# Optimization experiments

Measured on AMD Instinct MI355X. Metric: run time of the kernel, lower is better.

Reference implementation:

```python
import jax, jax.numpy as jnp
import numpy as np

DIM = 1024
HEADS = 16

def setup_inputs() -> dict:
    key = jax.random.key(0)
    ks = jax.random.split(key, 9)
    s = DIM ** -0.5  # init scale for weights
    x = jax.random.normal(ks[0], (2, 2048, DIM), dtype=jnp.float32)
    wq = jax.random.normal(ks[1], (DIM, DIM), dtype=jnp.float32) * s
    bq = jax.random.normal(ks[2], (DIM,), dtype=jnp.float32) * 0.01
    wk = jax.random.normal(ks[3], (DIM, DIM), dtype=jnp.float32) * s
    bk = jax.random.normal(ks[4], (DIM,), dtype=jnp.float32) * 0.01
    wv = jax.random.normal(ks[5], (DIM, DIM), dtype=jnp.float32) * s
    bv = jax.random.normal(ks[6], (DIM,), dtype=jnp.float32) * 0.01
    wo = jax.random.normal(ks[7], (DIM, DIM), dtype=jnp.float32) * s
    bo = jax.random.normal(ks[8], (DIM,), dtype=jnp.float32) * 0.01
    return {"x": x, "wq": wq, "bq": bq, "wk": wk, "bk": bk,
            "wv": wv, "bv": bv, "wo": wo, "bo": bo}

def reference(x, wq, bq, wk, bk, wv, bv, wo, bo):
    b, l, dim = x.shape
    h = HEADS
    d = dim // h
    scale = dim ** -0.5  # NOTE: full dim, as in the original module
    # torch Linear: x @ W.T + b
    def proj(w, bias):
        y = jnp.einsum('bld,ed->ble', x, w) + bias
        return y.reshape(b, l, h, d).transpose(0, 2, 1, 3)  # b h l d
    q = proj(wq, bq)
    k = proj(wk, bk)
    v = proj(wv, bv)
    attn = jnp.einsum('bhid,bhjd->bhij', q, k) * scale
    attn = jax.nn.softmax(attn, axis=-1)
    out = jnp.einsum('bhij,bhjd->bhid', attn, v)
    out = out.transpose(0, 2, 1, 3).reshape(b, l, dim)
    return jnp.einsum('ble,fe->blf', out, wo) + bo
```

## Files before the change

### kernel.cpp

```cpp
#include <hip/hip_runtime.h>
#include <hip/hip_bf16.h>
#include <stdint.h>


typedef __attribute__((ext_vector_type(8))) short short8;
typedef __attribute__((ext_vector_type(4))) float f32x4;
typedef __attribute__((ext_vector_type(16))) float f32x16;

#define MFMA(a, b, c) __builtin_amdgcn_mfma_f32_16x16x32_bf16((a), (b), (c), 0, 0, 0)
#define MFMA32(a, b, c) __builtin_amdgcn_mfma_f32_32x32x16_bf16((a), (b), (c), 0, 0, 0)

#if __has_builtin(__builtin_amdgcn_exp2f)
#define EXP2(x) __builtin_amdgcn_exp2f(x)
#else
#define EXP2(x) exp2f(x)
#endif

__device__ __forceinline__ ushort f2bf(float f) {
  uint32_t u = __builtin_bit_cast(uint32_t, f);
  u += 0x7fffu + ((u >> 16) & 1u);
  return (ushort)(u >> 16);
}

__device__ __forceinline__ uint32_t pkbf(float lo, float hi) {
  __hip_bfloat162 h = __float22bfloat162_rn(make_float2(lo, hi));
  uint32_t u;
  __builtin_memcpy(&u, &h, 4);
  return u;
}

__device__ __forceinline__ uint32_t cvtpk(float lo, float hi) {
  uint32_t u;
  asm("v_cvt_pk_bf16_f32 %0, %1, %2" : "=v"(u) : "v"(lo), "v"(hi));
  return u;
}

__device__ __forceinline__ void pl32swap(uint32_t& a, uint32_t& b) {
  asm("v_permlane32_swap_b32 %0, %1" : "+v"(a), "+v"(b));
}

__device__ __forceinline__ void gl_lds16(const void* g, void* l) {
  __builtin_amdgcn_global_load_lds(
      (const __attribute__((address_space(1))) unsigned int*)g,
      (__attribute__((address_space(3))) unsigned int*)l, 16, 0, 0);
}

__global__ __launch_bounds__(256) void convert_all(
    const float* __restrict__ x, const float* __restrict__ wq,
    const float* __restrict__ wk, const float* __restrict__ wv,
    const float* __restrict__ wo, ushort* __restrict__ dst) {
  size_t i4 = (size_t)blockIdx.x * 256 + threadIdx.x;
  size_t e = i4 * 4;
  const float* src; size_t off;
  if (e < 4194304u)      { src = x;  off = e; }
  else if (e < 5242880u) { src = wq; off = e - 4194304u; }
  else if (e < 6291456u) { src = wk; off = e - 5242880u; }
  else if (e < 7340032u) { src = wv; off = e - 6291456u; }
  else                   { src = wo; off = e - 7340032u; }
  float4 v = *(const float4*)(src + off);
  ushort4 o = { f2bf(v.x), f2bf(v.y), f2bf(v.z), f2bf(v.w) };
  *(ushort4*)(dst + e) = o;
}

__global__ __launch_bounds__(256) void gemm_qkv(
    const ushort* __restrict__ xb,
    const ushort* __restrict__ wqb, const ushort* __restrict__ wkb,
    const ushort* __restrict__ wvb,
    const float* __restrict__ bq_, const float* __restrict__ bk_,
    const float* __restrict__ bv_,
    ushort* __restrict__ qout, ushort* __restrict__ kout,
    ushort* __restrict__ vtout) {
  __shared__ __align__(16) ushort As[128 * 32];
  __shared__ __align__(16) ushort Bs[128 * 32];
  const int z = blockIdx.z;
  const int bn = blockIdx.x, bm = blockIdx.y;
  const int t = threadIdx.x;
  const int w = t >> 6, lane = t & 63;
  const int wr = w >> 1, wc = w & 1;
  const int l15 = lane & 15, l4 = lane >> 4;

  const ushort* wb = (z == 0) ? wqb : (z == 1 ? wkb : wvb);
  const float* bias = (z == 0) ? bq_ : (z == 1 ? bk_ : bv_);

  f32x4 acc[4][4] = {};

  for (int kt = 0; kt < 32; ++kt) {
    __syncthreads();
#pragma unroll
    for (int rr = 0; rr < 2; ++rr) {
      int c = t + rr * 256;
      int row = c >> 2, cin = c & 3;
      gl_lds16(xb + (bm * 128 + row) * 1024 + kt * 32 + cin * 8, (void*)&As[c * 8]);
      gl_lds16(wb + (bn * 128 + row) * 1024 + kt * 32 + cin * 8, (void*)&Bs[c * 8]);
    }
    __syncthreads();
    short8 af[4], bfr[4];
#pragma unroll
    for (int mf = 0; mf < 4; ++mf)
      af[mf] = *(const short8*)&As[(wr * 64 + mf * 16 + l15) * 32 + l4 * 8];
#pragma unroll
    for (int nf = 0; nf < 4; ++nf)
      bfr[nf] = *(const short8*)&Bs[(wc * 64 + nf * 16 + l15) * 32 + l4 * 8];
    __builtin_amdgcn_s_setprio(1);
#pragma unroll
    for (int mf = 0; mf < 4; ++mf)
#pragma unroll
      for (int nf = 0; nf < 4; ++nf)
        acc[mf][nf] = MFMA(af[mf], bfr[nf], acc[mf][nf]);
    __builtin_amdgcn_s_setprio(0);
  }

  const float qsc = 0.045084439f;
#pragma unroll
  for (int mf = 0; mf < 4; ++mf) {
#pragma unroll
    for (int nf = 0; nf < 4; ++nf) {
      int n = bn * 128 + wc * 64 + nf * 16 + l15;
      int m0 = bm * 128 + wr * 64 + mf * 16 + l4 * 4;
      float b = bias[n];
      float vals[4];
#pragma unroll
      for (int r = 0; r < 4; ++r) vals[r] = acc[mf][nf][r] + b;
      int bb = m0 >> 11, l0 = m0 & 2047;
      int h = n >> 6, d = n & 63;
      int bh = bb * 16 + h;
      if (z == 2) {
        *(uint2*)&vtout[(bh * 64 + d) * 2048 + l0] =
            make_uint2(pkbf(vals[0], vals[1]), pkbf(vals[2], vals[3]));
      } else if (z == 0) {
#pragma unroll
        for (int r = 0; r < 4; ++r)
          qout[(bh * 2048 + l0 + r) * 64 + d] = f2bf(vals[r] * qsc);
      } else {
#pragma unroll
        for (int r = 0; r < 4; ++r)
          kout[(bh * 2048 + l0 + r) * 64 + d] = f2bf(vals[r]);
      }
    }
  }
}

__global__ __launch_bounds__(256, 2) void attn(
    const ushort* __restrict__ qb, const ushort* __restrict__ kb,
    const ushort* __restrict__ vtb, ushort* __restrict__ aout) {
  __shared__ __align__(16) ushort Ks[4][64 * 64];
  __shared__ __align__(16) ushort Vs[4][64 * 64];
  const int bid = blockIdx.x;
  const int xcd = bid & 7, idx = bid >> 3;
  const int bh = xcd * 4 + (idx >> 4);
  const int it = idx & 15;
  const int t = threadIdx.x, w = t >> 6, lane = t & 63;
  const int l31 = lane & 31, hi = lane >> 5;
  const size_t kvbase = (size_t)bh * (2048 * 64);
  const int i0 = it * 128 + w * 32;

  const int c0 = t, c1 = t + 256;
  const int r0 = c0 >> 3, s0 = (c0 & 7) ^ (r0 & 7);
  const int r1 = c1 >> 3, s1 = (c1 & 7) ^ (r1 & 7);

#define STAGE(bufi, jts)                                                     \
  {                                                                          \
    const int j0s = (jts) * 64;                                              \
    gl_lds16(kb + kvbase + (size_t)(j0s + r0) * 64 + s0 * 8,                 \
             (void*)&Ks[bufi][c0 * 8]);                                      \
    gl_lds16(kb + kvbase + (size_t)(j0s + r1) * 64 + s1 * 8,                 \
             (void*)&Ks[bufi][c1 * 8]);                                      \
    gl_lds16(vtb + kvbase + (size_t)r0 * 2048 + j0s + s0 * 8,                \
             (void*)&Vs[bufi][c0 * 8]);                                      \
    gl_lds16(vtb + kvbase + (size_t)r1 * 2048 + j0s + s1 * 8,                \
             (void*)&Vs[bufi][c1 * 8]);                                      \
  }

#define QKSTEP(kbuf)                                                         \
  {                                                                          \
    const ushort* Kc = &Ks[kbuf][0];                                         \
    __builtin_amdgcn_s_setprio(1);                                           \
    _Pragma("unroll")                                                        \
    for (int ks = 0; ks < 4; ++ks) {                                         \
      int ck = (ks * 2 + hi) ^ swz;                                          \
      short8 a0 = *(const short8*)&Kc[l31 * 64 + ck * 8];                    \
      short8 a1 = *(const short8*)&Kc[(32 + l31) * 64 + ck * 8];             \
      st0 = MFMA32(a0, qf[ks], st0);                                         \
      st1 = MFMA32(a1, qf[ks], st1);                                         \
    }                                                                        \
    __builtin_amdgcn_s_setprio(0);                                           \
  }

  short8 qf[4];
#pragma unroll
  for (int ks = 0; ks < 4; ++ks)
    qf[ks] = *(const short8*)&qb[kvbase + (size_t)(i0 + l31) * 64 + ks * 16 + hi * 8];

  f32x16 ot0 = {}, ot1 = {};
  float ts0 = 0.f, ts1 = 0.f, ts2 = 0.f, ts3 = 0.f;
  const int swz = (l31 & 7);

  STAGE(0, 0);
  STAGE(1, 1);
  asm volatile("s_waitcnt vmcnt(4)" ::: "memory");
  __builtin_amdgcn_s_barrier();
  asm volatile("" ::: "memory");

  f32x16 st0 = {}, st1 = {};
  QKSTEP(0);

  for (int jt = 0; jt < 32; ++jt) {
    const int cur = jt & 3;
    STAGE((jt + 2) & 3, (jt + 2 < 32) ? (jt + 2) : 31);

    const ushort* Vc = &Vs[cur][0];
    short8 va0[4], va1[4];
#pragma unroll
    for (int b = 0; b < 4; ++b) {
      int cv = (b * 2 + hi) ^ swz;
      va0[b] = *(const short8*)&Vc[l31 * 64 + cv * 8];
      va1[b] = *(const short8*)&Vc[(32 + l31) * 64 + cv * 8];
    }

    f32x16 p0, p1;
#pragma unroll
    for (int r = 0; r < 16; r += 4) {
      p0[r] = EXP2(st0[r]);         ts0 += p0[r];
      p0[r + 1] = EXP2(st0[r + 1]); ts1 += p0[r + 1];
      p0[r + 2] = EXP2(st0[r + 2]); ts2 += p0[r + 2];
      p0[r + 3] = EXP2(st0[r + 3]); ts3 += p0[r + 3];
    }
#pragma unroll
    for (int r = 0; r < 16; r += 4) {
      p1[r] = EXP2(st1[r]);         ts0 += p1[r];
      p1[r + 1] = EXP2(st1[r + 1]); ts1 += p1[r + 1];
      p1[r + 2] = EXP2(st1[r + 2]); ts2 += p1[r + 2];
      p1[r + 3] = EXP2(st1[r + 3]); ts3 += p1[r + 3];
    }

    short8 pb[4];
#pragma unroll
    for (int b = 0; b < 4; ++b) {
      f32x16 pv = (b < 2) ? p0 : p1;
      const int R = 8 * (b & 1);
      uint32_t c01 = cvtpk(pv[R + 0], pv[R + 1]);
      uint32_t c23 = cvtpk(pv[R + 2], pv[R + 3]);
      uint32_t c45 = cvtpk(pv[R + 4], pv[R + 5]);
      uint32_t c67 = cvtpk(pv[R + 6], pv[R + 7]);
      pl32swap(c01, c45);
      pl32swap(c23, c67);
      union { uint32_t u[4]; short8 s; } pk;
      pk.u[0] = c01; pk.u[1] = c23; pk.u[2] = c45; pk.u[3] = c67;
      pb[b] = pk.s;
    }

    __builtin_amdgcn_s_setprio(1);
#pragma unroll
    for (int b = 0; b < 4; ++b) {
      ot0 = MFMA32(va0[b], pb[b], ot0);
      ot1 = MFMA32(va1[b], pb[b], ot1);
    }
    __builtin_amdgcn_s_setprio(0);

    asm volatile("s_waitcnt vmcnt(4)" ::: "memory");
    __builtin_amdgcn_s_barrier();
    asm volatile("" ::: "memory");

    if (jt < 31) {
#pragma unroll
      for (int r = 0; r < 16; ++r) { st0[r] = 0.f; st1[r] = 0.f; }
      QKSTEP((jt + 1) & 3);
    }
  }

  float lsum = (ts0 + ts1) + (ts2 + ts3);
  {
    uint32_t a = __builtin_bit_cast(uint32_t, lsum);
    uint32_t b = a;
    pl32swap(a, b);
    lsum = __builtin_bit_cast(float, a) + __builtin_bit_cast(float, b);
  }
  const int bb = bh >> 4, h = bh & 15;
  float inv = 1.0f / lsum;
  ushort* orow = aout + (size_t)(bb * 2048 + i0 + l31) * 1024 + h * 64;
#pragma unroll
  for (int mf = 0; mf < 2; ++mf) {
    f32x16 o = mf ? ot1 : ot0;
#pragma unroll
    for (int g = 0; g < 4; ++g) {
      int d0 = mf * 32 + g * 8 + hi * 4;
      *(uint2*)(orow + d0) = make_uint2(
          cvtpk(o[g * 4 + 0] * inv, o[g * 4 + 1] * inv),
          cvtpk(o[g * 4 + 2] * inv, o[g * 4 + 3] * inv));
    }
  }
#undef STAGE
#undef QKSTEP
}

__global__ __launch_bounds__(256) void gemm_out(
    const ushort* __restrict__ ab, const ushort* __restrict__ wob,
    const float* __restrict__ bo_, float* __restrict__ out) {
  __shared__ __align__(16) ushort As[128 * 32];
  __shared__ __align__(16) ushort Bs[128 * 32];
  const int bn = blockIdx.x, bm = blockIdx.y;
  const int t = threadIdx.x;
  const int w = t >> 6, lane = t & 63;
  const int wr = w >> 1, wc = w & 1;
  const int l15 = lane & 15, l4 = lane >> 4;

  f32x4 acc[4][4] = {};

  for (int kt = 0; kt < 32; ++kt) {
    __syncthreads();
#pragma unroll
    for (int rr = 0; rr < 2; ++rr) {
      int c = t + rr * 256;
      int row = c >> 2, cin = c & 3;
      gl_lds16(ab + (bm * 128 + row) * 1024 + kt * 32 + cin * 8, (void*)&As[c * 8]);
      gl_lds16(wob + (bn * 128 + row) * 1024 + kt * 32 + cin * 8, (void*)&Bs[c * 8]);
    }
    __syncthreads();
    short8 af[4], bfr[4];
#pragma unroll
    for (int mf = 0; mf < 4; ++mf)
      af[mf] = *(const short8*)&As[(wr * 64 + mf * 16 + l15) * 32 + l4 * 8];
#pragma unroll
    for (int nf = 0; nf < 4; ++nf)
      bfr[nf] = *(const short8*)&Bs[(wc * 64 + nf * 16 + l15) * 32 + l4 * 8];
    __builtin_amdgcn_s_setprio(1);
#pragma unroll
    for (int mf = 0; mf < 4; ++mf)
#pragma unroll
      for (int nf = 0; nf < 4; ++nf)
        acc[mf][nf] = MFMA(af[mf], bfr[nf], acc[mf][nf]);
    __builtin_amdgcn_s_setprio(0);
  }

#pragma unroll
  for (int mf = 0; mf < 4; ++mf)
#pragma unroll
    for (int nf = 0; nf < 4; ++nf) {
      int n = bn * 128 + wc * 64 + nf * 16 + l15;
      int m0 = bm * 128 + wr * 64 + mf * 16 + l4 * 4;
      float b = bo_[n];
#pragma unroll
      for (int r = 0; r < 4; ++r)
        out[(size_t)(m0 + r) * 1024 + n] = acc[mf][nf][r] + b;
    }
}

extern "C" void kernel_launch(void* const* d_in, const int* in_sizes, int n_in,
                              void* d_out, int out_size, void* d_ws, size_t ws_size,
                              hipStream_t stream) {
  const float* x  = (const float*)d_in[0];
  const float* wq = (const float*)d_in[1];
  const float* bq = (const float*)d_in[2];
  const float* wk = (const float*)d_in[3];
  const float* bk = (const float*)d_in[4];
  const float* wv = (const float*)d_in[5];
  const float* bv = (const float*)d_in[6];
  const float* wo = (const float*)d_in[7];
  const float* bo = (const float*)d_in[8];

  ushort* ws  = (ushort*)d_ws;
  ushort* xb  = ws;
  ushort* wqb = ws + 4194304;
  ushort* wkb = ws + 5242880;
  ushort* wvb = ws + 6291456;
  ushort* wob = ws + 7340032;
  ushort* qbp = ws + 8388608;
  ushort* kbp = ws + 12582912;
  ushort* vtb = ws + 16777216;
  ushort* ab  = ws + 20971520;

  convert_all<<<8192, 256, 0, stream>>>(x, wq, wk, wv, wo, ws);
  gemm_qkv<<<dim3(8, 32, 3), 256, 0, stream>>>(xb, wqb, wkb, wvb, bq, bk, bv,
                                               qbp, kbp, vtb);
  attn<<<512, 256, 0, stream>>>(qbp, kbp, vtb, ab);
  gemm_out<<<dim3(8, 32), 256, 0, stream>>>(ab, wob, bo, (float*)d_out);
}
```

Measured before the change: 112.6 us.

## Use 32x32 MFMA with K=64 swizzled LDS tiles in projection GEMMs

```diff
diff --git a/kernel.cpp b/kernel.cpp
--- a/kernel.cpp
+++ b/kernel.cpp
@@ -7,7 +7,6 @@
 typedef __attribute__((ext_vector_type(4))) float f32x4;
 typedef __attribute__((ext_vector_type(16))) float f32x16;
 
-#define MFMA(a, b, c) __builtin_amdgcn_mfma_f32_16x16x32_bf16((a), (b), (c), 0, 0, 0)
 #define MFMA32(a, b, c) __builtin_amdgcn_mfma_f32_32x32x16_bf16((a), (b), (c), 0, 0, 0)
 
 #if __has_builtin(__builtin_amdgcn_exp2f)
@@ -20,13 +19,6 @@
   uint32_t u = __builtin_bit_cast(uint32_t, f);
   u += 0x7fffu + ((u >> 16) & 1u);
   return (ushort)(u >> 16);
-}
-
-__device__ __forceinline__ uint32_t pkbf(float lo, float hi) {
-  __hip_bfloat162 h = __float22bfloat162_rn(make_float2(lo, hi));
-  uint32_t u;
-  __builtin_memcpy(&u, &h, 4);
-  return u;
 }
 
 __device__ __forceinline__ uint32_t cvtpk(float lo, float hi) {
@@ -70,71 +62,90 @@
     const float* __restrict__ bv_,
     ushort* __restrict__ qout, ushort* __restrict__ kout,
     ushort* __restrict__ vtout) {
-  __shared__ __align__(16) ushort As[128 * 32];
-  __shared__ __align__(16) ushort Bs[128 * 32];
+  __shared__ __align__(16) ushort As[128 * 64];
+  __shared__ __align__(16) ushort Bs[128 * 64];
   const int z = blockIdx.z;
   const int bn = blockIdx.x, bm = blockIdx.y;
   const int t = threadIdx.x;
   const int w = t >> 6, lane = t & 63;
   const int wr = w >> 1, wc = w & 1;
-  const int l15 = lane & 15, l4 = lane >> 4;
+  const int l31 = lane & 31, hi = lane >> 5;
+  const int swz = l31 & 7;
 
   const ushort* wb = (z == 0) ? wqb : (z == 1 ? wkb : wvb);
   const float* bias = (z == 0) ? bq_ : (z == 1 ? bk_ : bv_);
 
-  f32x4 acc[4][4] = {};
-
-  for (int kt = 0; kt < 32; ++kt) {
+  f32x16 acc[2][2] = {};
+
+  for (int kt = 0; kt < 16; ++kt) {
     __syncthreads();
 #pragma unroll
-    for (int rr = 0; rr < 2; ++rr) {
+    for (int rr = 0; rr < 4; ++rr) {
       int c = t + rr * 256;
-      int row = c >> 2, cin = c & 3;
-      gl_lds16(xb + (bm * 128 + row) * 1024 + kt * 32 + cin * 8, (void*)&As[c * 8]);
-      gl_lds16(wb + (bn * 128 + row) * 1024 + kt * 32 + cin * 8, (void*)&Bs[c * 8]);
+      int row = c >> 3, o = c & 7;
+      int sc = (o ^ (row & 7)) * 8;
+      gl_lds16(xb + (bm * 128 + row) * 1024 + kt * 64 + sc, (void*)&As[c * 8]);
+      gl_lds16(wb + (bn * 128 + row) * 1024 + kt * 64 + sc, (void*)&Bs[c * 8]);
     }
     __syncthreads();
-    short8 af[4], bfr[4];
-#pragma unroll
-    for (int mf = 0; mf < 4; ++mf)
-      af[mf] = *(const short8*)&As[(wr * 64 + mf * 16 + l15) * 32 + l4 * 8];
-#pragma unroll
-    for (int nf = 0; nf < 4; ++nf)
-      bfr[nf] = *(const short8*)&Bs[(wc * 64 + nf * 16 + l15) * 32 + l4 * 8];
+    short8 af[2][4], bf[2][4];
+#pragma unroll
+    for (int mb = 0; mb < 2; ++mb) {
+      int row = wr * 64 + mb * 32 + l31;
+#pragma unroll
+      for (int ks = 0; ks < 4; ++ks) {
+        int ck = (ks * 2 + hi) ^ swz;
+        af[mb][ks] = *(const short8*)&As[row * 64 + ck * 8];
+      }
+    }
+#pragma unroll
+    for (int nb = 0; nb < 2; ++nb) {
+      int row = wc * 64 + nb * 32 + l31;
+#pragma unroll
+      for (int ks = 0; ks < 4; ++ks) {
+        int ck = (ks * 2 + hi) ^ swz;
+        bf[nb][ks] = *(const short8*)&Bs[row * 64 + ck * 8];
+      }
+    }
     __builtin_amdgcn_s_setprio(1);
 #pragma unroll
-    for (int mf = 0; mf < 4; ++mf)
-#pragma unroll
-      for (int nf = 0; nf < 4; ++nf)
-        acc[mf][nf] = MFMA(af[mf], bfr[nf], acc[mf][nf]);
+    for (int ks = 0; ks < 4; ++ks)
+#pragma unroll
+      for (int mb = 0; mb < 2; ++mb)
+#pragma unroll
+        for (int nb = 0; nb < 2; ++nb)
+          acc[mb][nb] = MFMA32(af[mb][ks], bf[nb][ks], acc[mb][nb]);
     __builtin_amdgcn_s_setprio(0);
   }
 
   const float qsc = 0.045084439f;
 #pragma unroll
-  for (int mf = 0; mf < 4; ++mf) {
-#pragma unroll
-    for (int nf = 0; nf < 4; ++nf) {
-      int n = bn * 128 + wc * 64 + nf * 16 + l15;
-      int m0 = bm * 128 + wr * 64 + mf * 16 + l4 * 4;
+  for (int mb = 0; mb < 2; ++mb) {
+#pragma unroll
+    for (int nb = 0; nb < 2; ++nb) {
+      int n = bn * 128 + wc * 64 + nb * 32 + l31;
       float b = bias[n];
-      float vals[4];
-#pragma unroll
-      for (int r = 0; r < 4; ++r) vals[r] = acc[mf][nf][r] + b;
-      int bb = m0 >> 11, l0 = m0 & 2047;
       int h = n >> 6, d = n & 63;
-      int bh = bb * 16 + h;
-      if (z == 2) {
-        *(uint2*)&vtout[(bh * 64 + d) * 2048 + l0] =
-            make_uint2(pkbf(vals[0], vals[1]), pkbf(vals[2], vals[3]));
-      } else if (z == 0) {
-#pragma unroll
-        for (int r = 0; r < 4; ++r)
-          qout[(bh * 2048 + l0 + r) * 64 + d] = f2bf(vals[r] * qsc);
-      } else {
-#pragma unroll
-        for (int r = 0; r < 4; ++r)
-          kout[(bh * 2048 + l0 + r) * 64 + d] = f2bf(vals[r]);
+#pragma unroll
+      for (int g = 0; g < 4; ++g) {
+        int m0 = bm * 128 + wr * 64 + mb * 32 + g * 8 + hi * 4;
+        float vals[4];
+#pragma unroll
+        for (int e = 0; e < 4; ++e) vals[e] = acc[mb][nb][g * 4 + e] + b;
+        int bb = m0 >> 11, l0 = m0 & 2047;
+        int bh = bb * 16 + h;
+        if (z == 2) {
+          *(uint2*)&vtout[(bh * 64 + d) * 2048 + l0] =
+              make_uint2(cvtpk(vals[0], vals[1]), cvtpk(vals[2], vals[3]));
+        } else if (z == 0) {
+#pragma unroll
+          for (int e = 0; e < 4; ++e)
+            qout[(bh * 2048 + l0 + e) * 64 + d] = f2bf(vals[e] * qsc);
+        } else {
+#pragma unroll
+          for (int e = 0; e < 4; ++e)
+            kout[(bh * 2048 + l0 + e) * 64 + d] = f2bf(vals[e]);
+        }
       }
     }
   }
@@ -296,52 +307,71 @@
 __global__ __launch_bounds__(256) void gemm_out(
     const ushort* __restrict__ ab, const ushort* __restrict__ wob,
     const float* __restrict__ bo_, float* __restrict__ out) {
-  __shared__ __align__(16) ushort As[128 * 32];
-  __shared__ __align__(16) ushort Bs[128 * 32];
+  __shared__ __align__(16) ushort As[128 * 64];
+  __shared__ __align__(16) ushort Bs[128 * 64];
   const int bn = blockIdx.x, bm = blockIdx.y;
   const int t = threadIdx.x;
   const int w = t >> 6, lane = t & 63;
   const int wr = w >> 1, wc = w & 1;
-  const int l15 = lane & 15, l4 = lane >> 4;
-
-  f32x4 acc[4][4] = {};
-
-  for (int kt = 0; kt < 32; ++kt) {
+  const int l31 = lane & 31, hi = lane >> 5;
+  const int swz = l31 & 7;
+
+  f32x16 acc[2][2] = {};
+
+  for (int kt = 0; kt < 16; ++kt) {
     __syncthreads();
 #pragma unroll
-    for (int rr = 0; rr < 2; ++rr) {
+    for (int rr = 0; rr < 4; ++rr) {
       int c = t + rr * 256;
-      int row = c >> 2, cin = c & 3;
-      gl_lds16(ab + (bm * 128 + row) * 1024 + kt * 32 + cin * 8, (void*)&As[c * 8]);
-      gl_lds16(wob + (bn * 128 + row) * 1024 + kt * 32 + cin * 8, (void*)&Bs[c * 8]);
+      int row = c >> 3, o = c & 7;
+      int sc = (o ^ (row & 7)) * 8;
+      gl_lds16(ab + (bm * 128 + row) * 1024 + kt * 64 + sc, (void*)&As[c * 8]);
+      gl_lds16(wob + (bn * 128 + row) * 1024 + kt * 64 + sc, (void*)&Bs[c * 8]);
     }
     __syncthreads();
-    short8 af[4], bfr[4];
-#pragma unroll
-    for (int mf = 0; mf < 4; ++mf)
-      af[mf] = *(const short8*)&As[(wr * 64 + mf * 16 + l15) * 32 + l4 * 8];
-#pragma unroll
-    for (int nf = 0; nf < 4; ++nf)
-      bfr[nf] = *(const short8*)&Bs[(wc * 64 + nf * 16 + l15) * 32 + l4 * 8];
+    short8 af[2][4], bf[2][4];
+#pragma unroll
+    for (int mb = 0; mb < 2; ++mb) {
+      int row = wr * 64 + mb * 32 + l31;
+#pragma unroll
+      for (int ks = 0; ks < 4; ++ks) {
+        int ck = (ks * 2 + hi) ^ swz;
+        af[mb][ks] = *(const short8*)&As[row * 64 + ck * 8];
+      }
+    }
+#pragma unroll
+    for (int nb = 0; nb < 2; ++nb) {
+      int row = wc * 64 + nb * 32 + l31;
+#pragma unroll
+      for (int ks = 0; ks < 4; ++ks) {
+        int ck = (ks * 2 + hi) ^ swz;
+        bf[nb][ks] = *(const short8*)&Bs[row * 64 + ck * 8];
+      }
+    }
     __builtin_amdgcn_s_setprio(1);
 #pragma unroll
-    for (int mf = 0; mf < 4; ++mf)
-#pragma unroll
-      for (int nf = 0; nf < 4; ++nf)
-        acc[mf][nf] = MFMA(af[mf], bfr[nf], acc[mf][nf]);
+    for (int ks = 0; ks < 4; ++ks)
+#pragma unroll
+      for (int mb = 0; mb < 2; ++mb)
+#pragma unroll
+        for (int nb = 0; nb < 2; ++nb)
+          acc[mb][nb] = MFMA32(af[mb][ks], bf[nb][ks], acc[mb][nb]);
     __builtin_amdgcn_s_setprio(0);
   }
 
 #pragma unroll
-  for (int mf = 0; mf < 4; ++mf)
-#pragma unroll
-    for (int nf = 0; nf < 4; ++nf) {
-      int n = bn * 128 + wc * 64 + nf * 16 + l15;
-      int m0 = bm * 128 + wr * 64 + mf * 16 + l4 * 4;
+  for (int mb = 0; mb < 2; ++mb)
+#pragma unroll
+    for (int nb = 0; nb < 2; ++nb) {
+      int n = bn * 128 + wc * 64 + nb * 32 + l31;
       float b = bo_[n];
 #pragma unroll
-      for (int r = 0; r < 4; ++r)
-        out[(size_t)(m0 + r) * 1024 + n] = acc[mf][nf][r] + b;
+      for (int g = 0; g < 4; ++g) {
+        int m0 = bm * 128 + wr * 64 + mb * 32 + g * 8 + hi * 4;
+#pragma unroll
+        for (int e = 0; e < 4; ++e)
+          out[(size_t)(m0 + e) * 1024 + n] = acc[mb][nb][g * 4 + e] + b;
+      }
     }
 }
 
```

Measured after the change: 122.2 us. +8.5%, slower.

## Double-buffer LDS tiles in QKV and output projection GEMMs

Applied to the files above, without the earlier changes.

```diff
diff --git a/kernel.cpp b/kernel.cpp
--- a/kernel.cpp
+++ b/kernel.cpp
@@ -20,13 +20,6 @@
   uint32_t u = __builtin_bit_cast(uint32_t, f);
   u += 0x7fffu + ((u >> 16) & 1u);
   return (ushort)(u >> 16);
-}
-
-__device__ __forceinline__ uint32_t pkbf(float lo, float hi) {
-  __hip_bfloat162 h = __float22bfloat162_rn(make_float2(lo, hi));
-  uint32_t u;
-  __builtin_memcpy(&u, &h, 4);
-  return u;
 }
 
 __device__ __forceinline__ uint32_t cvtpk(float lo, float hi) {
@@ -70,8 +63,8 @@
     const float* __restrict__ bv_,
     ushort* __restrict__ qout, ushort* __restrict__ kout,
     ushort* __restrict__ vtout) {
-  __shared__ __align__(16) ushort As[128 * 32];
-  __shared__ __align__(16) ushort Bs[128 * 32];
+  __shared__ __align__(16) ushort As[2][128 * 32];
+  __shared__ __align__(16) ushort Bs[2][128 * 32];
   const int z = blockIdx.z;
   const int bn = blockIdx.x, bm = blockIdx.y;
   const int t = threadIdx.x;
@@ -82,25 +75,34 @@
   const ushort* wb = (z == 0) ? wqb : (z == 1 ? wkb : wvb);
   const float* bias = (z == 0) ? bq_ : (z == 1 ? bk_ : bv_);
 
+#define STAGEG(bufi, kts)                                                    \
+  {                                                                          \
+    _Pragma("unroll")                                                        \
+    for (int rr = 0; rr < 2; ++rr) {                                         \
+      int c = t + rr * 256;                                                  \
+      int row = c >> 2, cin = c & 3;                                         \
+      gl_lds16(xb + (bm * 128 + row) * 1024 + (kts) * 32 + cin * 8,          \
+               (void*)&As[bufi][c * 8]);                                     \
+      gl_lds16(wb + (bn * 128 + row) * 1024 + (kts) * 32 + cin * 8,          \
+               (void*)&Bs[bufi][c * 8]);                                     \
+    }                                                                        \
+  }
+
   f32x4 acc[4][4] = {};
 
+  STAGEG(0, 0);
+  __syncthreads();
+
   for (int kt = 0; kt < 32; ++kt) {
-    __syncthreads();
-#pragma unroll
-    for (int rr = 0; rr < 2; ++rr) {
-      int c = t + rr * 256;
-      int row = c >> 2, cin = c & 3;
-      gl_lds16(xb + (bm * 128 + row) * 1024 + kt * 32 + cin * 8, (void*)&As[c * 8]);
-      gl_lds16(wb + (bn * 128 + row) * 1024 + kt * 32 + cin * 8, (void*)&Bs[c * 8]);
-    }
-    __syncthreads();
+    const int cur = kt & 1;
+    if (kt < 31) STAGEG(cur ^ 1, kt + 1);
     short8 af[4], bfr[4];
 #pragma unroll
     for (int mf = 0; mf < 4; ++mf)
-      af[mf] = *(const short8*)&As[(wr * 64 + mf * 16 + l15) * 32 + l4 * 8];
+      af[mf] = *(const short8*)&As[cur][(wr * 64 + mf * 16 + l15) * 32 + l4 * 8];
 #pragma unroll
     for (int nf = 0; nf < 4; ++nf)
-      bfr[nf] = *(const short8*)&Bs[(wc * 64 + nf * 16 + l15) * 32 + l4 * 8];
+      bfr[nf] = *(const short8*)&Bs[cur][(wc * 64 + nf * 16 + l15) * 32 + l4 * 8];
     __builtin_amdgcn_s_setprio(1);
 #pragma unroll
     for (int mf = 0; mf < 4; ++mf)
@@ -108,6 +110,7 @@
       for (int nf = 0; nf < 4; ++nf)
         acc[mf][nf] = MFMA(af[mf], bfr[nf], acc[mf][nf]);
     __builtin_amdgcn_s_setprio(0);
+    __syncthreads();
   }
 
   const float qsc = 0.045084439f;
@@ -126,7 +129,7 @@
       int bh = bb * 16 + h;
       if (z == 2) {
         *(uint2*)&vtout[(bh * 64 + d) * 2048 + l0] =
-            make_uint2(pkbf(vals[0], vals[1]), pkbf(vals[2], vals[3]));
+            make_uint2(cvtpk(vals[0], vals[1]), cvtpk(vals[2], vals[3]));
       } else if (z == 0) {
 #pragma unroll
         for (int r = 0; r < 4; ++r)
@@ -138,6 +141,7 @@
       }
     }
   }
+#undef STAGEG
 }
 
 __global__ __launch_bounds__(256, 2) void attn(
@@ -296,33 +300,42 @@
 __global__ __launch_bounds__(256) void gemm_out(
     const ushort* __restrict__ ab, const ushort* __restrict__ wob,
     const float* __restrict__ bo_, float* __restrict__ out) {
-  __shared__ __align__(16) ushort As[128 * 32];
-  __shared__ __align__(16) ushort Bs[128 * 32];
+  __shared__ __align__(16) ushort As[2][128 * 32];
+  __shared__ __align__(16) ushort Bs[2][128 * 32];
   const int bn = blockIdx.x, bm = blockIdx.y;
   const int t = threadIdx.x;
   const int w = t >> 6, lane = t & 63;
   const int wr = w >> 1, wc = w & 1;
   const int l15 = lane & 15, l4 = lane >> 4;
 
+#define STAGEG(bufi, kts)                                                    \
+  {                                                                          \
+    _Pragma("unroll")                                                        \
+    for (int rr = 0; rr < 2; ++rr) {                                         \
+      int c = t + rr * 256;                                                  \
+      int row = c >> 2, cin = c & 3;                                         \
+      gl_lds16(ab + (bm * 128 + row) * 1024 + (kts) * 32 + cin * 8,          \
+               (void*)&As[bufi][c * 8]);                                     \
+      gl_lds16(wob + (bn * 128 + row) * 1024 + (kts) * 32 + cin * 8,         \
+               (void*)&Bs[bufi][c * 8]);                                     \
+    }                                                                        \
+  }
+
   f32x4 acc[4][4] = {};
 
+  STAGEG(0, 0);
+  __syncthreads();
+
   for (int kt = 0; kt < 32; ++kt) {
-    __syncthreads();
-#pragma unroll
-    for (int rr = 0; rr < 2; ++rr) {
-      int c = t + rr * 256;
-      int row = c >> 2, cin = c & 3;
-      gl_lds16(ab + (bm * 128 + row) * 1024 + kt * 32 + cin * 8, (void*)&As[c * 8]);
-      gl_lds16(wob + (bn * 128 + row) * 1024 + kt * 32 + cin * 8, (void*)&Bs[c * 8]);
-    }
-    __syncthreads();
+    const int cur = kt & 1;
+    if (kt < 31) STAGEG(cur ^ 1, kt + 1);
     short8 af[4], bfr[4];
 #pragma unroll
     for (int mf = 0; mf < 4; ++mf)
-      af[mf] = *(const short8*)&As[(wr * 64 + mf * 16 + l15) * 32 + l4 * 8];
+      af[mf] = *(const short8*)&As[cur][(wr * 64 + mf * 16 + l15) * 32 + l4 * 8];
 #pragma unroll
     for (int nf = 0; nf < 4; ++nf)
-      bfr[nf] = *(const short8*)&Bs[(wc * 64 + nf * 16 + l15) * 32 + l4 * 8];
+      bfr[nf] = *(const short8*)&Bs[cur][(wc * 64 + nf * 16 + l15) * 32 + l4 * 8];
     __builtin_amdgcn_s_setprio(1);
 #pragma unroll
     for (int mf = 0; mf < 4; ++mf)
@@ -330,6 +343,7 @@
       for (int nf = 0; nf < 4; ++nf)
         acc[mf][nf] = MFMA(af[mf], bfr[nf], acc[mf][nf]);
     __builtin_amdgcn_s_setprio(0);
+    __syncthreads();
   }
 
 #pragma unroll
@@ -343,6 +357,7 @@
       for (int r = 0; r < 4; ++r)
         out[(size_t)(m0 + r) * 1024 + n] = acc[mf][nf][r] + b;
     }
+#undef STAGEG
 }
 
 extern "C" void kernel_launch(void* const* d_in, const int* in_sizes, int n_in,
```

Measured after the change: 115.6 us. 1.03x slower.
